# Kernel tuning notes

Measured on AMD Instinct MI355X. Metric: run time of the kernel, lower is better.

## Reference

```python
import jax, jax.numpy as jnp
import numpy as np
import math

V, B, C, H, W = 4, 8, 512, 16, 16
NH = 8


def setup_inputs() -> dict:
    key = jax.random.key(0)
    ks = jax.random.split(key, 10)
    def n(k, shape, s=1.0):
        return jax.random.normal(k, shape, dtype=jnp.float32) * s
    return dict(
        i=n(ks[0], (V, B, C, H, W)),
        c=n(ks[1], (V, B, C, H, W)),
        j=n(ks[2], (V, B, C, H, W)),
        ln1_g=jnp.ones((C,), jnp.float32), ln1_b=jnp.zeros((C,), jnp.float32),
        ln2_g=jnp.ones((C,), jnp.float32), ln2_b=jnp.zeros((C,), jnp.float32),
        Wq=n(ks[3], (C, C), 0.02), bq=jnp.zeros((C,), jnp.float32),
        Wkv=n(ks[4], (C, 2 * C), 0.02), bkv=jnp.zeros((2 * C,), jnp.float32),
        Wo=n(ks[5], (C, C), 0.02), bo=jnp.zeros((C,), jnp.float32),
        Wfc=n(ks[6], (C, 4 * C), 0.02), bfc=jnp.zeros((4 * C,), jnp.float32),
        Wpr=n(ks[7], (4 * C, C), 0.02), bpr=jnp.zeros((C,), jnp.float32),
    )


def _ln(x, g, b, eps=1e-5):
    mu = jnp.mean(x, axis=-1, keepdims=True)
    var = jnp.mean((x - mu) ** 2, axis=-1, keepdims=True)
    return (x - mu) * jax.lax.rsqrt(var + eps) * g + b


def _gelu_new(x):
    # 0.5*x*(1+tanh(sqrt(2/pi)*(x+0.044715*x^3)))
    k = math.sqrt(2.0 / math.pi)
    return 0.5 * x * (1.0 + jnp.tanh(k * (x + 0.044715 * x ** 3)))


def reference(i, c, j, ln1_g, ln1_b, ln2_g, ln2_b, Wq, bq, Wkv, bkv, Wo, bo, Wfc, bfc, Wpr, bpr):
    v, b, ch, h, w = i.shape
    T = v * h * w
    hd = ch // NH

    def to_seq(x):  # v b c h w -> b (v h w) c
        return jnp.transpose(x, (1, 0, 3, 4, 2)).reshape(b, T, ch)

    # LayerNorm (over channel dim) applied before attention
    qs = _ln(to_seq(i), ln1_g, ln1_b)   # [b, T, c]
    kvs = _ln(to_seq(j), ln1_g, ln1_b)  # [b, T, c]

    q = qs @ Wq + bq                    # [b, T, c]
    kv = kvs @ Wkv + bkv                # [b, T, 2c]
    k, vv = jnp.split(kv, 2, axis=-1)

    def heads(x):  # [b, T, c] -> [b, nh, T, hd]
        return x.reshape(b, T, NH, hd).transpose(0, 2, 1, 3)
    q, k, vv = heads(q), heads(k), heads(vv)

    # block-causal mask: token in view-block r attends to view-blocks <= r
    blk = jnp.arange(T) // (h * w)
    mask = blk[:, None] >= blk[None, :]  # [T, T] bool

    att = jnp.einsum('bhqd,bhkd->bhqk', q, k) * (1.0 / math.sqrt(hd))
    att = jnp.where(mask, att, -jnp.inf)
    att = jax.nn.softmax(att, axis=-1)
    y = jnp.einsum('bhqk,bhkd->bhqd', att, vv)
    y = y.transpose(0, 2, 1, 3).reshape(b, T, ch)
    y = y @ Wo + bo                     # attention output, seq layout

    # residual: ln1(c) + attn
    cs = _ln(to_seq(c), ln1_g, ln1_b) + y
    # MLP with residual
    hcs = _ln(cs, ln2_g, ln2_b)
    cs = cs + (_gelu_new(hcs @ Wfc + bfc) @ Wpr + bpr)

    # b (v h w) c -> v b c h w
    out = cs.reshape(b, v, h, w, ch).transpose(1, 0, 4, 2, 3)
    return out
```

## Files before the change

kernel.cpp:

```cpp
#include <hip/hip_runtime.h>
#include <hip/hip_bf16.h>
#include <math.h>


typedef __bf16 bf16;
typedef __bf16 bf16x8 __attribute__((ext_vector_type(8)));
typedef __bf16 bf16x4 __attribute__((ext_vector_type(4)));
typedef float  f32x4  __attribute__((ext_vector_type(4)));

__device__ __forceinline__ void gload_lds16(const void* g, void* l) {
  __builtin_amdgcn_global_load_lds(
      (__attribute__((address_space(1))) void*)(g),
      (__attribute__((address_space(3))) void*)(l), 16, 0, 0);
}

__global__ __launch_bounds__(256)
void prep_w_k(const float* __restrict__ Wq, const float* __restrict__ Wkv,
              const float* __restrict__ Wo, const float* __restrict__ Wfc,
              const float* __restrict__ Wpr,
              bf16* __restrict__ WqT, bf16* __restrict__ WkvT,
              bf16* __restrict__ WoT, bf16* __restrict__ WfcT,
              bf16* __restrict__ WprT)
{
  __shared__ float tile[64 * 65];
  const int t = blockIdx.x;
  const int tid = threadIdx.x;
  const float* W; bf16* Wt; int K, N, nx, tl;
  if (t < 64)        { W = Wq;  Wt = WqT;  K = 512;  N = 512;  nx = 8;  tl = t; }
  else if (t < 192)  { W = Wkv; Wt = WkvT; K = 512;  N = 1024; nx = 16; tl = t - 64; }
  else if (t < 256)  { W = Wo;  Wt = WoT;  K = 512;  N = 512;  nx = 8;  tl = t - 192; }
  else if (t < 512)  { W = Wfc; Wt = WfcT; K = 512;  N = 2048; nx = 32; tl = t - 256; }
  else               { W = Wpr; Wt = WprT; K = 2048; N = 512;  nx = 8;  tl = t - 512; }
  const int bx = tl % nx, by = tl / nx;
  const int n0 = bx << 6, k0 = by << 6;

  const int xl = tid & 15, yl = tid >> 4;
#pragma unroll
  for (int r = 0; r < 4; ++r) {
    const int row = yl + r * 16;
    const f32x4 vv = *(const f32x4*)&W[(size_t)(k0 + row) * N + n0 + xl * 4];
#pragma unroll
    for (int e = 0; e < 4; ++e)
      tile[row * 65 + xl * 4 + e] = vv[e];
  }
  __syncthreads();
  const int xk = tid & 7, nl = tid >> 3;
#pragma unroll
  for (int r2 = 0; r2 < 2; ++r2) {
    const int n = nl + r2 * 32;
    bf16x8 o;
#pragma unroll
    for (int e = 0; e < 8; ++e)
      o[e] = (bf16)tile[(xk * 8 + e) * 65 + n];
    *(bf16x8*)&Wt[(size_t)(n0 + n) * K + k0 + xk * 8] = o;
  }
}

__global__ __launch_bounds__(256)
void prep_ln_k(const float* __restrict__ xi, const float* __restrict__ xj,
               const float* __restrict__ xc,
               const float* __restrict__ g, const float* __restrict__ bb,
               bf16* __restrict__ qs, bf16* __restrict__ kvs,
               bf16* __restrict__ csb)
{
  __shared__ __align__(16) float red[4][64];
  const int tid = threadIdx.x;
  const int u = blockIdx.x;
  const int sel = u >> 8, bid = u & 255;
  const int hp = bid & 7, b = (bid >> 3) & 7, v = bid >> 6;
  const float* src = (sel == 0) ? xi : ((sel == 1) ? xj : xc);
  const size_t base = ((size_t)(v * 8 + b) * 512) * 256 + hp * 32;
  const int q8 = tid & 7, chb = tid >> 3;
  const int wid = tid >> 6, lc = (tid >> 3) & 7;
  const int cb = chb << 4;

  float gr[16], br[16];
#pragma unroll
  for (int p = 0; p < 4; ++p) {
    *(f32x4*)&gr[p * 4] = *(const f32x4*)&g[cb + p * 4];
    *(f32x4*)&br[p * 4] = *(const f32x4*)&bb[cb + p * 4];
  }
  f32x4 x[16];
#pragma unroll
  for (int k = 0; k < 16; ++k)
    x[k] = *(const f32x4*)&src[base + (size_t)(cb + k) * 256 + q8 * 4];

  float s[4] = {0.f, 0.f, 0.f, 0.f}, ss[4] = {0.f, 0.f, 0.f, 0.f};
#pragma unroll
  for (int k = 0; k < 16; ++k)
#pragma unroll
    for (int i = 0; i < 4; ++i) {
      s[i] += x[k][i];
      ss[i] += x[k][i] * x[k][i];
    }
#pragma unroll
  for (int off = 8; off < 64; off <<= 1)
#pragma unroll
    for (int i = 0; i < 4; ++i) {
      s[i] += __shfl_xor(s[i], off);
      ss[i] += __shfl_xor(ss[i], off);
    }
  if (lc < 4)      red[wid][q8 * 4 + lc]      = s[lc];
  else             red[wid][32 + q8 * 4 + (lc - 4)] = ss[lc - 4];
  __syncthreads();
  f32x4 st = {0.f, 0.f, 0.f, 0.f}, sst = {0.f, 0.f, 0.f, 0.f};
#pragma unroll
  for (int w = 0; w < 4; ++w) {
    st  += *(const f32x4*)&red[w][q8 * 4];
    sst += *(const f32x4*)&red[w][32 + q8 * 4];
  }
  float mu[4], rs[4];
#pragma unroll
  for (int i = 0; i < 4; ++i) {
    mu[i] = st[i] * (1.f / 512.f);
    rs[i] = rsqrtf(sst[i] * (1.f / 512.f) - mu[i] * mu[i] + 1e-5f);
  }
  bf16* dstb = (sel == 0) ? qs : ((sel == 1) ? kvs : csb);
  const int tkb = v * 256 + hp * 32 + q8 * 4;
#pragma unroll
  for (int i = 0; i < 4; ++i) {
    const size_t orow = ((size_t)b * 1024 + tkb + i) * 512 + cb;
    bf16x8 o0, o1;
#pragma unroll
    for (int k = 0; k < 8; ++k) {
      o0[k] = (bf16)((x[k][i] - mu[i]) * rs[i] * gr[k] + br[k]);
      o1[k] = (bf16)((x[k + 8][i] - mu[i]) * rs[i] * gr[k + 8] + br[k + 8]);
    }
    *(bf16x8*)&dstb[orow]     = o0;
    *(bf16x8*)&dstb[orow + 8] = o1;
  }
}

__global__ __launch_bounds__(256)
void ln2_k(const bf16* __restrict__ cs, const float* __restrict__ g,
           const float* __restrict__ bb, bf16* __restrict__ hcs)
{
  const int tid = threadIdx.x, wid = tid >> 6, lane = tid & 63;
  const int row = blockIdx.x * 4 + wid;
  const bf16x8 v8 = *(const bf16x8*)&cs[(size_t)row * 512 + lane * 8];
  float v[8];
#pragma unroll
  for (int k = 0; k < 8; ++k) v[k] = (float)v8[k];
  float s = 0.f, ss = 0.f;
#pragma unroll
  for (int k = 0; k < 8; ++k) { s += v[k]; ss += v[k] * v[k]; }
#pragma unroll
  for (int off = 1; off < 64; off <<= 1) {
    s += __shfl_xor(s, off);
    ss += __shfl_xor(ss, off);
  }
  const float mu = s * (1.f / 512.f);
  const float rstd = rsqrtf(ss * (1.f / 512.f) - mu * mu + 1e-5f);
  bf16x8 o;
#pragma unroll
  for (int k = 0; k < 8; ++k) {
    int ch = lane * 8 + k;
    o[k] = (bf16)((v[k] - mu) * rstd * g[ch] + bb[ch]);
  }
  *(bf16x8*)&hcs[(size_t)row * 512 + lane * 8] = o;
}

__global__ __launch_bounds__(256)
void gemm_fc_k(const bf16* __restrict__ A, const bf16* __restrict__ Bt,
               const float* __restrict__ bias, bf16* __restrict__ fo)
{
  const int K = 512;
  __shared__ __align__(16) char smem[34816];
  bf16* As = (bf16*)smem;
  bf16* Bs = (bf16*)(smem + 16384);
  const int tid = threadIdx.x;
  const int wid = tid >> 6, lane = tid & 63;
  const int wr = wid >> 1, wc = wid & 1;
  const int ml = lane & 15, kg = (lane >> 4) << 3;
  const int m0 = blockIdx.x * 128, n0 = blockIdx.y * 128;

  const int e0 = wid * 512 + lane * 8;
  const int r0 = e0 >> 5, c0 = e0 & 31;
  const int e1 = e0 + 2048;
  const int r1 = e1 >> 5, c1 = e1 & 31;

  const bf16* Ag = A + (size_t)m0 * K;
  const bf16* Bg = Bt + (size_t)n0 * K;

  f32x4 acc[4][4] = {};

  gload_lds16(Ag + (size_t)r0 * K + c0, As + wid * 512);
  gload_lds16(Ag + (size_t)r1 * K + c1, As + 2048 + wid * 512);
  gload_lds16(Bg + (size_t)r0 * K + c0, Bs + wid * 512);
  gload_lds16(Bg + (size_t)r1 * K + c1, Bs + 2048 + wid * 512);

  int cur = 0;
  for (int k0 = 0; k0 < K; k0 += 32) {
    __syncthreads();
    if (k0 + 32 < K) {
      const int nb = cur ^ 1, kn = k0 + 32;
      gload_lds16(Ag + (size_t)r0 * K + kn + c0, As + nb * 4096 + wid * 512);
      gload_lds16(Ag + (size_t)r1 * K + kn + c1, As + nb * 4096 + 2048 + wid * 512);
      gload_lds16(Bg + (size_t)r0 * K + kn + c0, Bs + nb * 4096 + wid * 512);
      gload_lds16(Bg + (size_t)r1 * K + kn + c1, Bs + nb * 4096 + 2048 + wid * 512);
    }
    bf16x8 af[4], bfr[4];
#pragma unroll
    for (int mf = 0; mf < 4; ++mf)
      af[mf] = *(const bf16x8*)&As[cur * 4096 + (wr * 64 + mf * 16 + ml) * 32 + kg];
#pragma unroll
    for (int nf = 0; nf < 4; ++nf)
      bfr[nf] = *(const bf16x8*)&Bs[cur * 4096 + (wc * 64 + nf * 16 + ml) * 32 + kg];
#pragma unroll
    for (int mf = 0; mf < 4; ++mf)
#pragma unroll
      for (int nf = 0; nf < 4; ++nf)
        acc[mf][nf] = __builtin_amdgcn_mfma_f32_16x16x32_bf16(
            af[mf], bfr[nf], acc[mf][nf], 0, 0, 0);
    cur ^= 1;
  }

  __syncthreads();
  bf16* OT = (bf16*)smem;
  const int jrow0 = (lane >> 4) << 2;
#pragma unroll
  for (int nf = 0; nf < 4; ++nf) {
    const float bv = bias[n0 + wc * 64 + nf * 16 + ml];
#pragma unroll
    for (int mf = 0; mf < 4; ++mf)
#pragma unroll
      for (int j = 0; j < 4; ++j) {
        float x = acc[mf][nf][j] + bv;
        float u = 0.7978845608f * (x + 0.044715f * x * x * x);
        float e = __expf(2.f * u);
        float th = 1.f - 2.f / (e + 1.f);
        OT[(wr * 64 + mf * 16 + jrow0 + j) * 132 + wc * 64 + nf * 16 + ml] =
            (bf16)(0.5f * x * (1.f + th));
      }
  }
  __syncthreads();
#pragma unroll
  for (int it = 0; it < 8; ++it) {
    const int idx = it * 256 + tid;
    const int cg = idx & 15, r = idx >> 4;
    *(bf16x8*)&fo[(size_t)(m0 + r) * 2048 + n0 + cg * 8] =
        *(const bf16x8*)&OT[r * 132 + cg * 8];
  }
}

enum { EPI_O = 2, EPI_PR = 4 };

template <int EPI>
__global__ __launch_bounds__(512)
void gemmsk_k(const bf16* __restrict__ A, const bf16* __restrict__ Bt,
              const float* __restrict__ bias, const bf16* res,
              void* out0, int K)
{
  __shared__ __align__(16) char smem[49152];
  bf16*  AS = (bf16*)smem;
  bf16*  BS = (bf16*)(smem + 16384);
  float* CF = (float*)smem;

  const int tid = threadIdx.x;
  const int wid = tid >> 6, lane = tid & 63;
  const int half = wid >> 2, w2 = wid & 3;
  const int wr = w2 >> 1, wc = w2 & 1;
  const int ml = lane & 15, kg = (lane >> 4) << 3;
  const int m0 = blockIdx.x * 64, n0 = blockIdx.y * 128;
  const int Kh = K >> 1;

  const int eA = w2 * 512 + lane * 8;
  const int rA = eA >> 5, cA = eA & 31;
  const int eB0 = (w2 * 2) * 512 + lane * 8;
  const int rB0 = eB0 >> 5, cB0 = eB0 & 31;
  const int eB1 = eB0 + 512;
  const int rB1 = eB1 >> 5, cB1 = eB1 & 31;

  const bf16* Ag = A + (size_t)m0 * K + half * Kh;
  const bf16* Bg = Bt + (size_t)n0 * K + half * Kh;

  f32x4 acc[2][4] = {};

  gload_lds16(Ag + (size_t)rA * K + cA, AS + half * 2048 + w2 * 512);
  gload_lds16(Bg + (size_t)rB0 * K + cB0, BS + half * 4096 + (w2 * 2) * 512);
  gload_lds16(Bg + (size_t)rB1 * K + cB1, BS + half * 4096 + (w2 * 2 + 1) * 512);

  int cur = 0;
  for (int k0 = 0; k0 < Kh; k0 += 32) {
    __syncthreads();
    if (k0 + 32 < Kh) {
      const int kn = k0 + 32, nb = cur ^ 1;
      gload_lds16(Ag + (size_t)rA * K + kn + cA,
                  AS + nb * 4096 + half * 2048 + w2 * 512);
      gload_lds16(Bg + (size_t)rB0 * K + kn + cB0,
                  BS + nb * 8192 + half * 4096 + (w2 * 2) * 512);
      gload_lds16(Bg + (size_t)rB1 * K + kn + cB1,
                  BS + nb * 8192 + half * 4096 + (w2 * 2 + 1) * 512);
    }
    const bf16* Ac = AS + cur * 4096 + half * 2048;
    const bf16* Bc = BS + cur * 8192 + half * 4096;
    bf16x8 af[2], bfr[4];
#pragma unroll
    for (int mf = 0; mf < 2; ++mf)
      af[mf] = *(const bf16x8*)&Ac[(wr * 32 + mf * 16 + ml) * 32 + kg];
#pragma unroll
    for (int nf = 0; nf < 4; ++nf)
      bfr[nf] = *(const bf16x8*)&Bc[(wc * 64 + nf * 16 + ml) * 32 + kg];
#pragma unroll
    for (int mf = 0; mf < 2; ++mf)
#pragma unroll
      for (int nf = 0; nf < 4; ++nf)
        acc[mf][nf] = __builtin_amdgcn_mfma_f32_16x16x32_bf16(
            af[mf], bfr[nf], acc[mf][nf], 0, 0, 0);
    cur ^= 1;
  }

  const int jrow0 = (lane >> 4) << 2;
  __syncthreads();
  if (half == 0) {
#pragma unroll
    for (int mf = 0; mf < 2; ++mf)
#pragma unroll
      for (int nf = 0; nf < 4; ++nf)
#pragma unroll
        for (int j = 0; j < 4; ++j)
          CF[(wr * 32 + mf * 16 + jrow0 + j) * 128 + wc * 64 + nf * 16 + ml] =
              acc[mf][nf][j];
  }
  __syncthreads();
  if (half == 1) {
#pragma unroll
    for (int nf = 0; nf < 4; ++nf) {
      const int n = n0 + wc * 64 + nf * 16 + ml;
      const float bv = bias[n];
#pragma unroll
      for (int mf = 0; mf < 2; ++mf) {
        const int mbase = m0 + wr * 32 + mf * 16 + jrow0;
        float v4[4];
#pragma unroll
        for (int j = 0; j < 4; ++j)
          v4[j] = acc[mf][nf][j] +
                  CF[(wr * 32 + mf * 16 + jrow0 + j) * 128 + wc * 64 + nf * 16 + ml];
        if constexpr (EPI == EPI_O) {
          bf16* cs = (bf16*)out0;
#pragma unroll
          for (int j = 0; j < 4; ++j) {
            const size_t idx = (size_t)(mbase + j) * 512 + n;
            cs[idx] = (bf16)(v4[j] + bv + (float)res[idx]);
          }
        } else {
          float* out = (float*)out0;
          const int b = mbase >> 10, t = mbase & 1023;
          const int v = t >> 8, hhh = (t >> 4) & 15, w0 = t & 15;
          f32x4 o;
#pragma unroll
          for (int j = 0; j < 4; ++j)
            o[j] = v4[j] + bv + (float)res[(size_t)(mbase + j) * 512 + n];
          *(f32x4*)&out[(((size_t)v * 8 + b) * 512 + n) * 256 + hhh * 16 + w0] = o;
        }
      }
    }
  }
}

__global__ __launch_bounds__(256)
void gemm_qkv_k(const bf16* __restrict__ Aq, const bf16* __restrict__ Akv,
                const bf16* __restrict__ WqT, const bf16* __restrict__ WkvT,
                const float* __restrict__ bq, const float* __restrict__ bkv,
                bf16* __restrict__ q_buf, bf16* __restrict__ k_buf,
                bf16* __restrict__ v_t)
{
  const int K = 512;
  __shared__ __align__(16) char smem[34816];
  bf16* As = (bf16*)smem;
  bf16* Bs = (bf16*)(smem + 16384);
  const int tid = threadIdx.x;
  const int wid = tid >> 6, lane = tid & 63;
  const int wr = wid >> 1, wc = wid & 1;
  const int ml = lane & 15, kg = (lane >> 4) << 3;
  const int ybl = blockIdx.y;
  const bool isq = ybl < 4;
  const bf16* A     = isq ? Aq  : Akv;
  const bf16* Bt    = isq ? WqT : WkvT;
  const float* bias = isq ? bq : bkv;
  const int n0 = isq ? (ybl << 7) : ((ybl - 4) << 7);
  const int m0 = blockIdx.x * 128;

  const int e0 = wid * 512 + lane * 8;
  const int r0 = e0 >> 5, c0 = e0 & 31;
  const int e1 = e0 + 2048;
  const int r1 = e1 >> 5, c1 = e1 & 31;

  const bf16* Ag = A + (size_t)m0 * K;
  const bf16* Bg = Bt + (size_t)n0 * K;

  f32x4 acc[4][4] = {};

  gload_lds16(Ag + (size_t)r0 * K + c0, As + wid * 512);
  gload_lds16(Ag + (size_t)r1 * K + c1, As + 2048 + wid * 512);
  gload_lds16(Bg + (size_t)r0 * K + c0, Bs + wid * 512);
  gload_lds16(Bg + (size_t)r1 * K + c1, Bs + 2048 + wid * 512);

  int cur = 0;
  for (int k0 = 0; k0 < K; k0 += 32) {
    __syncthreads();
    if (k0 + 32 < K) {
      const int nb = cur ^ 1, kn = k0 + 32;
      gload_lds16(Ag + (size_t)r0 * K + kn + c0, As + nb * 4096 + wid * 512);
      gload_lds16(Ag + (size_t)r1 * K + kn + c1, As + nb * 4096 + 2048 + wid * 512);
      gload_lds16(Bg + (size_t)r0 * K + kn + c0, Bs + nb * 4096 + wid * 512);
      gload_lds16(Bg + (size_t)r1 * K + kn + c1, Bs + nb * 4096 + 2048 + wid * 512);
    }
    bf16x8 af[4], bfr[4];
#pragma unroll
    for (int mf = 0; mf < 4; ++mf)
      af[mf] = *(const bf16x8*)&As[cur * 4096 + (wr * 64 + mf * 16 + ml) * 32 + kg];
#pragma unroll
    for (int nf = 0; nf < 4; ++nf)
      bfr[nf] = *(const bf16x8*)&Bs[cur * 4096 + (wc * 64 + nf * 16 + ml) * 32 + kg];
#pragma unroll
    for (int mf = 0; mf < 4; ++mf)
#pragma unroll
      for (int nf = 0; nf < 4; ++nf)
        acc[mf][nf] = __builtin_amdgcn_mfma_f32_16x16x32_bf16(
            af[mf], bfr[nf], acc[mf][nf], 0, 0, 0);
    cur ^= 1;
  }

  __syncthreads();
  bf16* OT = (bf16*)smem;
  const int jrow0 = (lane >> 4) << 2;
  const int b = m0 >> 10, t0 = m0 & 1023;
  if (ybl < 8) {
#pragma unroll
    for (int nf = 0; nf < 4; ++nf) {
      const float bv = bias[n0 + wc * 64 + nf * 16 + ml];
#pragma unroll
      for (int mf = 0; mf < 4; ++mf)
#pragma unroll
        for (int j = 0; j < 4; ++j)
          OT[(wr * 64 + mf * 16 + jrow0 + j) * 132 + wc * 64 + nf * 16 + ml] =
              (bf16)(acc[mf][nf][j] + bv);
    }
    __syncthreads();
    bf16* dst = isq ? q_buf : k_buf;
    const int h0 = n0 >> 6;
#pragma unroll
    for (int it = 0; it < 8; ++it) {
      const int idx = it * 256 + tid;
      const int dg = idx & 7, r = (idx >> 3) & 127, hl = idx >> 10;
      *(bf16x8*)&dst[(((size_t)b * 8 + h0 + hl) * 1024 + t0 + r) * 64 + dg * 8] =
          *(const bf16x8*)&OT[r * 132 + hl * 64 + dg * 8];
    }
  } else {
#pragma unroll
    for (int nf = 0; nf < 4; ++nf) {
      const float bv = bias[n0 + wc * 64 + nf * 16 + ml];
#pragma unroll
      for (int mf = 0; mf < 4; ++mf) {
        bf16x4 o;
#pragma unroll
        for (int j = 0; j < 4; ++j) o[j] = (bf16)(acc[mf][nf][j] + bv);
        *(bf16x4*)&OT[(wc * 64 + nf * 16 + ml) * 132 + wr * 64 + mf * 16 + jrow0] = o;
      }
    }
    __syncthreads();
    const int h0 = (n0 - 512) >> 6;
#pragma unroll
    for (int it = 0; it < 8; ++it) {
      const int idx = it * 256 + tid;
      const int og = idx & 15, c = idx >> 4;
      const int hl = c >> 6, d = c & 63;
      *(bf16x8*)&v_t[(((size_t)b * 8 + h0 + hl) * 64 + d) * 1024 + t0 + og * 8] =
          *(const bf16x8*)&OT[c * 132 + og * 8];
    }
  }
}

__global__ __launch_bounds__(256)
void attn_k(const bf16* __restrict__ qb, const bf16* __restrict__ kb,
            const bf16* __restrict__ vt, bf16* __restrict__ y)
{
  __shared__ bf16 Ks[2][4096];
  __shared__ bf16 Vs[2][4096];
  __shared__ bf16 Ps[4][1024];
  const int tid = threadIdx.x, wid = tid >> 6, lane = tid & 63;
  const int L = blockIdx.x;
  const int xcd = L & 7, chunk = L >> 3;
  const int bh = xcd + ((chunk >> 4) << 3);
  const int qt = 15 - (chunk & 15);
  const int b = bh >> 3, h = bh & 7;
  const int t0 = qt << 6;
  const int ml = lane & 15, hi = lane >> 4, kg = hi << 3;

  const bf16* qrow = qb + ((size_t)bh * 1024 + t0 + wid * 16) * 64;
  bf16x8 aq[2];
  aq[0] = *(const bf16x8*)&qrow[ml * 64 + kg];
  aq[1] = *(const bf16x8*)&qrow[ml * 64 + 32 + kg];

  f32x4 accO[4] = {};
  float lsum[4] = {0.f, 0.f, 0.f, 0.f};

  const int nkt = ((qt >> 2) + 1) << 2;
  const bf16* kbase = kb + (size_t)bh * 1024 * 64;
  const bf16* vbase = vt + (size_t)bh * 64 * 1024;

  const int sr = (wid << 3) + (lane >> 3);
  const int sg = ((lane & 7) ^ ((lane >> 3) & 7)) << 3;
  bf16* pw = &Ps[wid][0];

  {
    gload_lds16(kbase + (size_t)sr * 64 + sg,          &Ks[0][wid * 512]);
    gload_lds16(kbase + (size_t)(sr + 32) * 64 + sg,   &Ks[0][2048 + wid * 512]);
    gload_lds16(vbase + (size_t)sr * 1024 + sg,        &Vs[0][wid * 512]);
    gload_lds16(vbase + (size_t)(sr + 32) * 1024 + sg, &Vs[0][2048 + wid * 512]);
  }

  int cur = 0;
  for (int kt = 0; kt < nkt; ++kt) {
    __syncthreads();
    if (kt + 1 < nkt) {
      const int tk0 = (kt + 1) << 6;
      const int nb = cur ^ 1;
      gload_lds16(kbase + (size_t)(tk0 + sr) * 64 + sg,        &Ks[nb][wid * 512]);
      gload_lds16(kbase + (size_t)(tk0 + sr + 32) * 64 + sg,   &Ks[nb][2048 + wid * 512]);
      gload_lds16(vbase + (size_t)sr * 1024 + tk0 + sg,        &Vs[nb][wid * 512]);
      gload_lds16(vbase + (size_t)(sr + 32) * 1024 + tk0 + sg, &Vs[nb][2048 + wid * 512]);
    }

    f32x4 sa[4] = {};
    __builtin_amdgcn_s_setprio(1);
#pragma unroll
    for (int nf = 0; nf < 4; ++nf) {
      const int row = nf * 16 + ml;
#pragma unroll
      for (int ks = 0; ks < 2; ++ks) {
        const int g = ((ks * 4 + hi) ^ (ml & 7)) << 3;
        bf16x8 bk = *(const bf16x8*)&Ks[cur][row * 64 + g];
        sa[nf] = __builtin_amdgcn_mfma_f32_16x16x32_bf16(aq[ks], bk, sa[nf], 0, 0, 0);
      }
    }
    __builtin_amdgcn_s_setprio(0);

#pragma unroll
    for (int nf = 0; nf < 4; ++nf) {
      const int gp0 = nf * 2 + (ml >> 3);
#pragma unroll
      for (int j = 0; j < 4; ++j) {
        const float p = __expf(sa[nf][j] * 0.125f);
        lsum[j] += p;
        const int prow = (hi << 2) + j;
        pw[prow * 64 + ((gp0 ^ (prow & 7)) << 3) + (ml & 7)] = (bf16)p;
      }
    }

    __builtin_amdgcn_s_setprio(1);
#pragma unroll
    for (int ks = 0; ks < 2; ++ks) {
      const int g = ((ks * 4 + hi) ^ (ml & 7)) << 3;
      bf16x8 pa = *(const bf16x8*)&pw[ml * 64 + g];
#pragma unroll
      for (int df = 0; df < 4; ++df) {
        bf16x8 bv = *(const bf16x8*)&Vs[cur][(df * 16 + ml) * 64 + g];
        accO[df] = __builtin_amdgcn_mfma_f32_16x16x32_bf16(pa, bv, accO[df], 0, 0, 0);
      }
    }
    __builtin_amdgcn_s_setprio(0);
    cur ^= 1;
  }

  float inv[4];
#pragma unroll
  for (int j = 0; j < 4; ++j) {
    float s = lsum[j];
#pragma unroll
    for (int off = 1; off < 16; off <<= 1) s += __shfl_xor(s, off);
    inv[j] = 1.f / s;
  }
#pragma unroll
  for (int df = 0; df < 4; ++df)
#pragma unroll
    for (int j = 0; j < 4; ++j) {
      const int t = t0 + wid * 16 + (hi << 2) + j;
      const int c = h * 64 + df * 16 + ml;
      y[((size_t)b * 1024 + t) * 512 + c] = (bf16)(accO[df][j] * inv[j]);
    }
}

extern "C" void kernel_launch(void* const* d_in, const int* in_sizes, int n_in,
                              void* d_out, int out_size, void* d_ws, size_t ws_size,
                              hipStream_t stream)
{
  const float* xi    = (const float*)d_in[0];
  const float* xc    = (const float*)d_in[1];
  const float* xj    = (const float*)d_in[2];
  const float* ln1_g = (const float*)d_in[3];
  const float* ln1_b = (const float*)d_in[4];
  const float* ln2_g = (const float*)d_in[5];
  const float* ln2_b = (const float*)d_in[6];
  const float* Wq    = (const float*)d_in[7];
  const float* bq    = (const float*)d_in[8];
  const float* Wkv   = (const float*)d_in[9];
  const float* bkv   = (const float*)d_in[10];
  const float* Wo    = (const float*)d_in[11];
  const float* bo    = (const float*)d_in[12];
  const float* Wfc   = (const float*)d_in[13];
  const float* bfc   = (const float*)d_in[14];
  const float* Wpr   = (const float*)d_in[15];
  const float* bpr   = (const float*)d_in[16];

  char* ws = (char*)d_ws;
  const size_t MB = 1ull << 20;
  bf16*  qs    = (bf16*)(ws + 0);
  bf16*  kvs   = (bf16*)(ws + 8 * MB);
  bf16*  csb   = (bf16*)(ws + 16 * MB);
  bf16*  WqT   = (bf16*)(ws + 32 * MB);
  bf16*  WkvT  = (bf16*)(ws + 32 * MB + 512 * 1024);
  bf16*  WoT   = (bf16*)(ws + 33 * MB + 512 * 1024);
  bf16*  WfcT  = (bf16*)(ws + 34 * MB);
  bf16*  WprT  = (bf16*)(ws + 36 * MB);
  bf16*  q_buf = (bf16*)(ws + 38 * MB);
  bf16*  k_buf = (bf16*)(ws + 46 * MB);
  bf16*  v_t   = (bf16*)(ws + 54 * MB);
  bf16*  yb    = (bf16*)(ws + 0);
  bf16*  hcs   = (bf16*)(ws + 8 * MB);
  bf16*  fcact = (bf16*)(ws + 38 * MB);

  prep_w_k<<<dim3(768), 256, 0, stream>>>(Wq, Wkv, Wo, Wfc, Wpr,
                                          WqT, WkvT, WoT, WfcT, WprT);
  prep_ln_k<<<dim3(768), 256, 0, stream>>>(xi, xj, xc, ln1_g, ln1_b,
                                           qs, kvs, csb);

  gemm_qkv_k<<<dim3(64, 12), 256, 0, stream>>>(qs, kvs, WqT, WkvT, bq, bkv,
                                               q_buf, k_buf, v_t);

  attn_k<<<dim3(1024), 256, 0, stream>>>(q_buf, k_buf, v_t, yb);

  gemmsk_k<EPI_O><<<dim3(128, 4), 512, 0, stream>>>(yb, WoT, bo, csb,
                                                    (void*)csb, 512);

  ln2_k<<<dim3(2048), 256, 0, stream>>>(csb, ln2_g, ln2_b, hcs);

  gemm_fc_k<<<dim3(64, 16), 256, 0, stream>>>(hcs, WfcT, bfc, fcact);

  gemmsk_k<EPI_PR><<<dim3(128, 4), 512, 0, stream>>>(fcact, WprT, bpr, csb,
                                                     d_out, 2048);

  (void)in_sizes; (void)n_in; (void)out_size; (void)ws_size;
}
```

Measured before the change: 162.6 us.

## Merge weight and LN prep kernels; widen attention tile to 128 queries

The two preprocessing kernels (weight transpose-to-bf16 and LayerNorm-to-bf16) are merged into one launch, with block index selecting which role a block plays. This removes one kernel launch and lets the two independent jobs share the GPU. The attention kernel now uses 512 threads (8 waves) per block and handles 128 query rows, so each K/V tile loaded into LDS serves twice as many queries and the grid halves. The tradeoff is coarser causal granularity and more LDS per block, which may reduce occupancy and add a little wasted masked work.

```diff
diff --git a/kernel.cpp b/kernel.cpp
--- a/kernel.cpp
+++ b/kernel.cpp
@@ -15,57 +15,54 @@
 }
 
 __global__ __launch_bounds__(256)
-void prep_w_k(const float* __restrict__ Wq, const float* __restrict__ Wkv,
-              const float* __restrict__ Wo, const float* __restrict__ Wfc,
-              const float* __restrict__ Wpr,
-              bf16* __restrict__ WqT, bf16* __restrict__ WkvT,
-              bf16* __restrict__ WoT, bf16* __restrict__ WfcT,
-              bf16* __restrict__ WprT)
+void prep_k(const float* __restrict__ Wq, const float* __restrict__ Wkv,
+            const float* __restrict__ Wo, const float* __restrict__ Wfc,
+            const float* __restrict__ Wpr,
+            bf16* __restrict__ WqT, bf16* __restrict__ WkvT,
+            bf16* __restrict__ WoT, bf16* __restrict__ WfcT,
+            bf16* __restrict__ WprT,
+            const float* __restrict__ xi, const float* __restrict__ xj,
+            const float* __restrict__ xc,
+            const float* __restrict__ g, const float* __restrict__ bb,
+            bf16* __restrict__ qs, bf16* __restrict__ kvs,
+            bf16* __restrict__ csb)
 {
   __shared__ float tile[64 * 65];
+  __shared__ float red[4][64];
   const int t = blockIdx.x;
   const int tid = threadIdx.x;
-  const float* W; bf16* Wt; int K, N, nx, tl;
-  if (t < 64)        { W = Wq;  Wt = WqT;  K = 512;  N = 512;  nx = 8;  tl = t; }
-  else if (t < 192)  { W = Wkv; Wt = WkvT; K = 512;  N = 1024; nx = 16; tl = t - 64; }
-  else if (t < 256)  { W = Wo;  Wt = WoT;  K = 512;  N = 512;  nx = 8;  tl = t - 192; }
-  else if (t < 512)  { W = Wfc; Wt = WfcT; K = 512;  N = 2048; nx = 32; tl = t - 256; }
-  else               { W = Wpr; Wt = WprT; K = 2048; N = 512;  nx = 8;  tl = t - 512; }
-  const int bx = tl % nx, by = tl / nx;
-  const int n0 = bx << 6, k0 = by << 6;
-
-  const int xl = tid & 15, yl = tid >> 4;
-#pragma unroll
-  for (int r = 0; r < 4; ++r) {
-    const int row = yl + r * 16;
-    const f32x4 vv = *(const f32x4*)&W[(size_t)(k0 + row) * N + n0 + xl * 4];
-#pragma unroll
-    for (int e = 0; e < 4; ++e)
-      tile[row * 65 + xl * 4 + e] = vv[e];
-  }
-  __syncthreads();
-  const int xk = tid & 7, nl = tid >> 3;
-#pragma unroll
-  for (int r2 = 0; r2 < 2; ++r2) {
-    const int n = nl + r2 * 32;
-    bf16x8 o;
-#pragma unroll
-    for (int e = 0; e < 8; ++e)
-      o[e] = (bf16)tile[(xk * 8 + e) * 65 + n];
-    *(bf16x8*)&Wt[(size_t)(n0 + n) * K + k0 + xk * 8] = o;
-  }
-}
-
-__global__ __launch_bounds__(256)
-void prep_ln_k(const float* __restrict__ xi, const float* __restrict__ xj,
-               const float* __restrict__ xc,
-               const float* __restrict__ g, const float* __restrict__ bb,
-               bf16* __restrict__ qs, bf16* __restrict__ kvs,
-               bf16* __restrict__ csb)
-{
-  __shared__ __align__(16) float red[4][64];
-  const int tid = threadIdx.x;
-  const int u = blockIdx.x;
+  if (t < 768) {
+    const float* W; bf16* Wt; int K, N, nx, tl;
+    if (t < 64)        { W = Wq;  Wt = WqT;  K = 512;  N = 512;  nx = 8;  tl = t; }
+    else if (t < 192)  { W = Wkv; Wt = WkvT; K = 512;  N = 1024; nx = 16; tl = t - 64; }
+    else if (t < 256)  { W = Wo;  Wt = WoT;  K = 512;  N = 512;  nx = 8;  tl = t - 192; }
+    else if (t < 512)  { W = Wfc; Wt = WfcT; K = 512;  N = 2048; nx = 32; tl = t - 256; }
+    else               { W = Wpr; Wt = WprT; K = 2048; N = 512;  nx = 8;  tl = t - 512; }
+    const int bx = tl % nx, by = tl / nx;
+    const int n0 = bx << 6, k0 = by << 6;
+    const int xl = tid & 15, yl = tid >> 4;
+#pragma unroll
+    for (int r = 0; r < 4; ++r) {
+      const int row = yl + r * 16;
+      const f32x4 vv = *(const f32x4*)&W[(size_t)(k0 + row) * N + n0 + xl * 4];
+#pragma unroll
+      for (int e = 0; e < 4; ++e)
+        tile[row * 65 + xl * 4 + e] = vv[e];
+    }
+    __syncthreads();
+    const int xk = tid & 7, nl = tid >> 3;
+#pragma unroll
+    for (int r2 = 0; r2 < 2; ++r2) {
+      const int n = nl + r2 * 32;
+      bf16x8 o;
+#pragma unroll
+      for (int e = 0; e < 8; ++e)
+        o[e] = (bf16)tile[(xk * 8 + e) * 65 + n];
+      *(bf16x8*)&Wt[(size_t)(n0 + n) * K + k0 + xk * 8] = o;
+    }
+    return;
+  }
+  const int u = t - 768;
   const int sel = u >> 8, bid = u & 255;
   const int hp = bid & 7, b = (bid >> 3) & 7, v = bid >> 6;
   const float* src = (sel == 0) ? xi : ((sel == 1) ? xj : xc);
@@ -100,7 +97,7 @@
       s[i] += __shfl_xor(s[i], off);
       ss[i] += __shfl_xor(ss[i], off);
     }
-  if (lc < 4)      red[wid][q8 * 4 + lc]      = s[lc];
+  if (lc < 4)      red[wid][q8 * 4 + lc]            = s[lc];
   else             red[wid][32 + q8 * 4 + (lc - 4)] = ss[lc - 4];
   __syncthreads();
   f32x4 st = {0.f, 0.f, 0.f, 0.f}, sst = {0.f, 0.f, 0.f, 0.f};
@@ -472,20 +469,20 @@
   }
 }
 
-__global__ __launch_bounds__(256)
+__global__ __launch_bounds__(512)
 void attn_k(const bf16* __restrict__ qb, const bf16* __restrict__ kb,
             const bf16* __restrict__ vt, bf16* __restrict__ y)
 {
   __shared__ bf16 Ks[2][4096];
   __shared__ bf16 Vs[2][4096];
-  __shared__ bf16 Ps[4][1024];
+  __shared__ bf16 Ps[8][1024];
   const int tid = threadIdx.x, wid = tid >> 6, lane = tid & 63;
   const int L = blockIdx.x;
   const int xcd = L & 7, chunk = L >> 3;
-  const int bh = xcd + ((chunk >> 4) << 3);
-  const int qt = 15 - (chunk & 15);
+  const int bh = xcd + ((chunk >> 3) << 3);
+  const int qt = 7 - (chunk & 7);
   const int b = bh >> 3, h = bh & 7;
-  const int t0 = qt << 6;
+  const int t0 = qt << 7;
   const int ml = lane & 15, hi = lane >> 4, kg = hi << 3;
 
   const bf16* qrow = qb + ((size_t)bh * 1024 + t0 + wid * 16) * 64;
@@ -496,20 +493,16 @@
   f32x4 accO[4] = {};
   float lsum[4] = {0.f, 0.f, 0.f, 0.f};
 
-  const int nkt = ((qt >> 2) + 1) << 2;
+  const int nkt = ((qt >> 1) + 1) << 2;
   const bf16* kbase = kb + (size_t)bh * 1024 * 64;
   const bf16* vbase = vt + (size_t)bh * 64 * 1024;
 
-  const int sr = (wid << 3) + (lane >> 3);
-  const int sg = ((lane & 7) ^ ((lane >> 3) & 7)) << 3;
+  const int sr = tid >> 3;
+  const int sg = ((tid & 7) ^ (sr & 7)) << 3;
   bf16* pw = &Ps[wid][0];
 
-  {
-    gload_lds16(kbase + (size_t)sr * 64 + sg,          &Ks[0][wid * 512]);
-    gload_lds16(kbase + (size_t)(sr + 32) * 64 + sg,   &Ks[0][2048 + wid * 512]);
-    gload_lds16(vbase + (size_t)sr * 1024 + sg,        &Vs[0][wid * 512]);
-    gload_lds16(vbase + (size_t)(sr + 32) * 1024 + sg, &Vs[0][2048 + wid * 512]);
-  }
+  gload_lds16(kbase + (size_t)sr * 64 + sg,   &Ks[0][wid * 512]);
+  gload_lds16(vbase + (size_t)sr * 1024 + sg, &Vs[0][wid * 512]);
 
   int cur = 0;
   for (int kt = 0; kt < nkt; ++kt) {
@@ -517,10 +510,8 @@
     if (kt + 1 < nkt) {
       const int tk0 = (kt + 1) << 6;
       const int nb = cur ^ 1;
-      gload_lds16(kbase + (size_t)(tk0 + sr) * 64 + sg,        &Ks[nb][wid * 512]);
-      gload_lds16(kbase + (size_t)(tk0 + sr + 32) * 64 + sg,   &Ks[nb][2048 + wid * 512]);
-      gload_lds16(vbase + (size_t)sr * 1024 + tk0 + sg,        &Vs[nb][wid * 512]);
-      gload_lds16(vbase + (size_t)(sr + 32) * 1024 + tk0 + sg, &Vs[nb][2048 + wid * 512]);
+      gload_lds16(kbase + (size_t)(tk0 + sr) * 64 + sg,   &Ks[nb][wid * 512]);
+      gload_lds16(vbase + (size_t)sr * 1024 + tk0 + sg,   &Vs[nb][wid * 512]);
     }
 
     f32x4 sa[4] = {};
@@ -621,15 +612,14 @@
   bf16*  hcs   = (bf16*)(ws + 8 * MB);
   bf16*  fcact = (bf16*)(ws + 38 * MB);
 
-  prep_w_k<<<dim3(768), 256, 0, stream>>>(Wq, Wkv, Wo, Wfc, Wpr,
-                                          WqT, WkvT, WoT, WfcT, WprT);
-  prep_ln_k<<<dim3(768), 256, 0, stream>>>(xi, xj, xc, ln1_g, ln1_b,
-                                           qs, kvs, csb);
+  prep_k<<<dim3(1536), 256, 0, stream>>>(Wq, Wkv, Wo, Wfc, Wpr,
+                                         WqT, WkvT, WoT, WfcT, WprT,
+                                         xi, xj, xc, ln1_g, ln1_b, qs, kvs, csb);
 
   gemm_qkv_k<<<dim3(64, 12), 256, 0, stream>>>(qs, kvs, WqT, WkvT, bq, bkv,
                                                q_buf, k_buf, v_t);
 
-  attn_k<<<dim3(1024), 256, 0, stream>>>(q_buf, k_buf, v_t, yb);
+  attn_k<<<dim3(512), 512, 0, stream>>>(q_buf, k_buf, v_t, yb);
 
   gemmsk_k<EPI_O><<<dim3(128, 4), 512, 0, stream>>>(yb, WoT, bo, csb,
                                                     (void*)csb, 512);
```

Result: faster. 155.2 us (-4.5%).
